# Kernel tuning notes

Measured on AMD Instinct MI355X. Metric: run time of the kernel, lower is better.

Reference implementation:

```python
import jax, jax.numpy as jnp
import numpy as np

N_EMBD = 1024
COND = 1024
N_HEAD = 16
B, N, NTOK = 4, 2048, 2048


def setup_inputs() -> dict:
    key = jax.random.key(0)
    ks = jax.random.split(key, 10)
    s = 0.02
    return {
        "x": jax.random.normal(ks[0], (B, N, N_EMBD), jnp.float32),
        "encoder_output": jax.random.normal(ks[1], (B, NTOK, COND), jnp.float32),
        "Wq": jax.random.normal(ks[2], (N_EMBD, N_EMBD), jnp.float32) * s,
        "bq": jnp.zeros((N_EMBD,), jnp.float32),
        "Wk": jax.random.normal(ks[3], (N_EMBD, COND), jnp.float32) * s,
        "bk": jnp.zeros((N_EMBD,), jnp.float32),
        "Wv": jax.random.normal(ks[4], (N_EMBD, COND), jnp.float32) * s,
        "bv": jnp.zeros((N_EMBD,), jnp.float32),
        "Wp": jax.random.normal(ks[5], (N_EMBD, N_EMBD), jnp.float32) * s,
        "bp": jnp.zeros((N_EMBD,), jnp.float32),
    }


def reference(x, encoder_output, Wq, bq, Wk, bk, Wv, bv, Wp, bp):
    Bx, Nx, C = x.shape
    H = N_HEAD
    D = C // H
    # projections (torch Linear: y = x @ W^T + b)
    q = (x @ Wq.T + bq).reshape(Bx, Nx, H, D)               # b n h d
    k = (encoder_output @ Wk.T + bk).reshape(Bx, -1, H, D)  # b t h d
    v = (encoder_output @ Wv.T + bv).reshape(Bx, -1, H, D)
    scale = 1.0 / jnp.sqrt(jnp.asarray(D, x.dtype))
    att = jnp.einsum("bnhd,bthd->bhnt", q, k) * scale
    att = jax.nn.softmax(att, axis=-1)
    y = jnp.einsum("bhnt,bthd->bnhd", att, v).reshape(Bx, Nx, C)
    y = y @ Wp.T + bp  # dropout is identity at inference (p effectively 0)
    return y
```

## Files before the change

kernel.cpp:

```cpp
#include <hip/hip_runtime.h>

typedef short bf16x8 __attribute__((ext_vector_type(8)));
typedef float f32x4 __attribute__((ext_vector_type(4)));
typedef unsigned int u32x2 __attribute__((ext_vector_type(2)));

#define AS1 __attribute__((address_space(1)))
#define AS3 __attribute__((address_space(3)))

__device__ __forceinline__ void gld16(void* lds, const void* g) {
  __builtin_amdgcn_global_load_lds((const AS1 unsigned int*)g,
                                   (AS3 unsigned int*)lds, 16, 0, 0);
}

__device__ __forceinline__ unsigned short f2bf(float f) {
  union { float f; unsigned int u; } c; c.f = f;
  return (unsigned short)((c.u + 0x7FFFu + ((c.u >> 16) & 1u)) >> 16);
}

__device__ __forceinline__ unsigned int cvtpk(float lo, float hi) {
  unsigned int r;
  asm("v_cvt_pk_bf16_f32 %0, %1, %2" : "=v"(r) : "v"(lo), "v"(hi));
  return r;
}

__global__ void cvt_kernel(const float4* __restrict__ in0,
                           const float4* __restrict__ in1,
                           ushort4* __restrict__ out0,
                           ushort4* __restrict__ out1, int n4) {
  const float4* in = blockIdx.y ? in1 : in0;
  ushort4* out = blockIdx.y ? out1 : out0;
  int i = blockIdx.x * blockDim.x + threadIdx.x;
  int stride = gridDim.x * blockDim.x;
  for (; i < n4; i += stride) {
    float4 v = in[i];
    ushort4 o;
    o.x = f2bf(v.x); o.y = f2bf(v.y); o.z = f2bf(v.z); o.w = f2bf(v.w);
    out[i] = o;
  }
}

__global__ void cvtw_kernel(const float4* w0, const float4* w1,
                            const float4* w2, const float4* w3,
                            ushort4* o0, ushort4* o1, ushort4* o2, ushort4* o3,
                            int n4) {
  const float4* in; ushort4* out;
  switch (blockIdx.y) {
    case 0: in = w0; out = o0; break;
    case 1: in = w1; out = o1; break;
    case 2: in = w2; out = o2; break;
    default: in = w3; out = o3; break;
  }
  int i = blockIdx.x * blockDim.x + threadIdx.x;
  int stride = gridDim.x * blockDim.x;
  for (; i < n4; i += stride) {
    float4 v = in[i];
    ushort4 o;
    o.x = f2bf(v.x); o.y = f2bf(v.y); o.z = f2bf(v.z); o.w = f2bf(v.w);
    out[i] = o;
  }
}

__global__ __launch_bounds__(256) void gemm_qkv_kernel(
    const unsigned short* __restrict__ Xb,
    const unsigned short* __restrict__ Eb,
    const unsigned short* __restrict__ Wqb,
    const unsigned short* __restrict__ Wkb,
    const unsigned short* __restrict__ Wvb,
    const float* __restrict__ bq,
    const float* __restrict__ bk,
    const float* __restrict__ bv,
    unsigned short* __restrict__ Qw,
    unsigned short* __restrict__ Kw,
    unsigned short* __restrict__ VTw,
    float qscale)
{
  __shared__ alignas(16) unsigned short As[2][4 * 128 * 8];
  __shared__ alignas(16) unsigned short Bs[2][4 * 128 * 8];

  const int sec = blockIdx.x >> 3;
  const int bx = blockIdx.x & 7;
  const unsigned short* A = (sec == 0) ? Xb : Eb;
  const unsigned short* W = (sec == 0) ? Wqb : (sec == 1) ? Wkb : Wvb;
  const float* bias = (sec == 0) ? bq : (sec == 1) ? bk : bv;

  const int K = 1024, N = 1024;
  const int tid = threadIdx.x;
  const int lane = tid & 63;
  const int w = tid >> 6;
  const int wr = (w >> 1) * 64;
  const int wc = (w & 1) * 64;
  const int lrow = lane & 15;
  const int lk = lane >> 4;
  const long m0 = (long)blockIdx.y * 128;
  const long n0 = (long)bx * 128;

  f32x4 acc[4][4] = {};

  const int c0 = tid, c1 = tid + 256;
  const unsigned short* Ag0 = A + (m0 + (c0 & 127)) * (long)K + (c0 >> 7) * 8;
  const unsigned short* Ag1 = A + (m0 + (c1 & 127)) * (long)K + (c1 >> 7) * 8;
  const unsigned short* Wg0 = W + (n0 + (c0 & 127)) * (long)K + (c0 >> 7) * 8;
  const unsigned short* Wg1 = W + (n0 + (c1 & 127)) * (long)K + (c1 >> 7) * 8;

  const int arow = wr + lrow;
  const int brow = wc + lrow;
  const int nt = K >> 5;

  gld16(As[0] + c0 * 8, Ag0);
  gld16(As[0] + c1 * 8, Ag1);
  gld16(Bs[0] + c0 * 8, Wg0);
  gld16(Bs[0] + c1 * 8, Wg1);

  int cur = 0;
  for (int t = 0; t < nt; ++t) {
    __syncthreads();
    if (t + 1 < nt) {
      const int kt = (t + 1) * 32;
      gld16(As[cur ^ 1] + c0 * 8, Ag0 + kt);
      gld16(As[cur ^ 1] + c1 * 8, Ag1 + kt);
      gld16(Bs[cur ^ 1] + c0 * 8, Wg0 + kt);
      gld16(Bs[cur ^ 1] + c1 * 8, Wg1 + kt);
    }
    const unsigned short* as = As[cur];
    const unsigned short* bs = Bs[cur];
    bf16x8 af[4], bfr[4];
#pragma unroll
    for (int i = 0; i < 4; ++i)
      af[i] = *(const bf16x8*)(as + (lk * 128 + arow + i * 16) * 8);
#pragma unroll
    for (int j = 0; j < 4; ++j)
      bfr[j] = *(const bf16x8*)(bs + (lk * 128 + brow + j * 16) * 8);
    if (sec != 2) {
#pragma unroll
      for (int i = 0; i < 4; ++i)
#pragma unroll
        for (int j = 0; j < 4; ++j)
          acc[i][j] = __builtin_amdgcn_mfma_f32_16x16x32_bf16(af[i], bfr[j], acc[i][j], 0, 0, 0);
    } else {
#pragma unroll
      for (int i = 0; i < 4; ++i)
#pragma unroll
        for (int j = 0; j < 4; ++j)
          acc[i][j] = __builtin_amdgcn_mfma_f32_16x16x32_bf16(bfr[i], af[j], acc[i][j], 0, 0, 0);
    }
    cur ^= 1;
  }

  if (sec != 2) {
    unsigned short* out = (sec == 0) ? Qw : Kw;
    const float scale = (sec == 0) ? qscale : 1.0f;
#pragma unroll
    for (int j = 0; j < 4; ++j) {
      const long col = n0 + wc + j * 16 + lrow;
      const float bv_ = bias[col];
#pragma unroll
      for (int i = 0; i < 4; ++i)
#pragma unroll
        for (int r = 0; r < 4; ++r) {
          const long row = m0 + wr + i * 16 + lk * 4 + r;
          out[row * (long)N + col] = f2bf((acc[i][j][r] + bv_) * scale);
        }
    }
  } else {
#pragma unroll
    for (int i = 0; i < 4; ++i)
#pragma unroll
      for (int r = 0; r < 4; ++r) {
        const long feat = n0 + wc + i * 16 + lk * 4 + r;
        const float bv_ = bias[feat];
#pragma unroll
        for (int j = 0; j < 4; ++j) {
          const long col = m0 + wr + j * 16 + lrow;
          VTw[feat * 8192 + col] = f2bf(acc[i][j][r] + bv_);
        }
      }
  }
}

__global__ __launch_bounds__(256) void gemm_bt_kernel(
    const unsigned short* __restrict__ A,
    const unsigned short* __restrict__ W,
    const float* __restrict__ bias,
    float* __restrict__ outF,
    int M, int N, int K)
{
  __shared__ alignas(16) unsigned short As[2][4 * 128 * 8];
  __shared__ alignas(16) unsigned short Bs[2][4 * 128 * 8];

  const int tid = threadIdx.x;
  const int lane = tid & 63;
  const int w = tid >> 6;
  const int wr = (w >> 1) * 64;
  const int wc = (w & 1) * 64;
  const int lrow = lane & 15;
  const int lk = lane >> 4;
  const long m0 = (long)blockIdx.y * 128;
  const long n0 = (long)blockIdx.x * 128;

  f32x4 acc[4][4] = {};

  const int c0 = tid, c1 = tid + 256;
  const unsigned short* Ag0 = A + (m0 + (c0 & 127)) * (long)K + (c0 >> 7) * 8;
  const unsigned short* Ag1 = A + (m0 + (c1 & 127)) * (long)K + (c1 >> 7) * 8;
  const unsigned short* Wg0 = W + (n0 + (c0 & 127)) * (long)K + (c0 >> 7) * 8;
  const unsigned short* Wg1 = W + (n0 + (c1 & 127)) * (long)K + (c1 >> 7) * 8;

  const int arow = wr + lrow;
  const int brow = wc + lrow;
  const int nt = K >> 5;

  gld16(As[0] + c0 * 8, Ag0);
  gld16(As[0] + c1 * 8, Ag1);
  gld16(Bs[0] + c0 * 8, Wg0);
  gld16(Bs[0] + c1 * 8, Wg1);

  int cur = 0;
  for (int t = 0; t < nt; ++t) {
    __syncthreads();
    if (t + 1 < nt) {
      const int kt = (t + 1) * 32;
      gld16(As[cur ^ 1] + c0 * 8, Ag0 + kt);
      gld16(As[cur ^ 1] + c1 * 8, Ag1 + kt);
      gld16(Bs[cur ^ 1] + c0 * 8, Wg0 + kt);
      gld16(Bs[cur ^ 1] + c1 * 8, Wg1 + kt);
    }
    const unsigned short* as = As[cur];
    const unsigned short* bs = Bs[cur];
    bf16x8 af[4], bfr[4];
#pragma unroll
    for (int i = 0; i < 4; ++i)
      af[i] = *(const bf16x8*)(as + (lk * 128 + arow + i * 16) * 8);
#pragma unroll
    for (int j = 0; j < 4; ++j)
      bfr[j] = *(const bf16x8*)(bs + (lk * 128 + brow + j * 16) * 8);
#pragma unroll
    for (int i = 0; i < 4; ++i)
#pragma unroll
      for (int j = 0; j < 4; ++j)
        acc[i][j] = __builtin_amdgcn_mfma_f32_16x16x32_bf16(af[i], bfr[j], acc[i][j], 0, 0, 0);
    cur ^= 1;
  }

#pragma unroll
  for (int j = 0; j < 4; ++j) {
    const long col = n0 + wc + j * 16 + lrow;
    const float bv_ = bias[col];
#pragma unroll
    for (int i = 0; i < 4; ++i)
#pragma unroll
      for (int r = 0; r < 4; ++r) {
        const long row = m0 + wr + i * 16 + lk * 4 + r;
        outF[row * (long)N + col] = acc[i][j][r] + bv_;
      }
  }
}

__global__ __launch_bounds__(256) void attn_kernel(
    const unsigned short* __restrict__ Q,
    const unsigned short* __restrict__ K,
    const unsigned short* __restrict__ VT,
    unsigned short* __restrict__ Y)
{
  __shared__ alignas(16) unsigned short Ks[2][8 * 64 * 8];
  __shared__ alignas(16) unsigned short Vt[2][64 * 64];
  __shared__ alignas(16) unsigned short Ps[128 * 72];

  const int tid = threadIdx.x;
  const int lane = tid & 63;
  const int w = tid >> 6;
  const int lrow = lane & 15;
  const int lk = lane >> 4;

  const int id = blockIdx.x;
  const int r8 = id & 7;
  const int s5 = id >> 3;
  const int qt = s5 & 15;
  const int bh = r8 + 8 * (s5 >> 4);
  const int h = bh & 15, b = bh >> 4;
  const long C = 1024, T = 2048, NQ = 2048;

  const unsigned short* Qg = Q + ((long)b * NQ + qt * 128) * C + h * 64;
  const unsigned short* Kg0 = K + (long)b * T * C + h * 64;
  const unsigned short* Vg0 = VT + (long)(h * 64) * 8192 + b * 2048;

  {
    int c = tid;
    gld16(Ks[0] + c * 8, Kg0 + (long)(c & 63) * C + (c >> 6) * 8);
    c = tid + 256;
    gld16(Ks[0] + c * 8, Kg0 + (long)(c & 63) * C + (c >> 6) * 8);
    c = tid;
    gld16(Vt[0] + c * 8, Vg0 + (long)(c >> 3) * 8192 + (((c & 7) ^ ((c >> 3) & 7)) * 8));
    c = tid + 256;
    gld16(Vt[0] + c * 8, Vg0 + (long)(c >> 3) * 8192 + (((c & 7) ^ ((c >> 3) & 7)) * 8));
  }
  bf16x8 qf[2][2];
#pragma unroll
  for (int f = 0; f < 2; ++f)
#pragma unroll
    for (int kk = 0; kk < 2; ++kk)
      qf[f][kk] = *(const bf16x8*)(Qg + (long)(f * 64 + w * 16 + lrow) * C + (kk * 4 + lk) * 8);

  bf16x8 ones;
#pragma unroll
  for (int e = 0; e < 8; ++e) ones[e] = (short)0x3F80;

  __syncthreads();

  f32x4 oA[4] = {}, oB[4] = {};
  f32x4 olA = {}, olB = {};
  float mrA = -1e30f, mrB = -1e30f;
  int cur = 0;

  const int qrow0 = w * 16 + lrow;

  for (int kt = 0; kt < (int)T; kt += 64) {
    const bool more = (kt + 64 < (int)T);
    if (more) {
      int c = tid;
      gld16(Ks[cur ^ 1] + c * 8, Kg0 + (long)(kt + 64 + (c & 63)) * C + (c >> 6) * 8);
      gld16(Vt[cur ^ 1] + c * 8,
            Vg0 + (long)(c >> 3) * 8192 + kt + 64 + (((c & 7) ^ ((c >> 3) & 7)) * 8));
      c = tid + 256;
      gld16(Ks[cur ^ 1] + c * 8, Kg0 + (long)(kt + 64 + (c & 63)) * C + (c >> 6) * 8);
      gld16(Vt[cur ^ 1] + c * 8,
            Vg0 + (long)(c >> 3) * 8192 + kt + 64 + (((c & 7) ^ ((c >> 3) & 7)) * 8));
    }

    f32x4 sA[4] = {}, sB[4] = {};
    __builtin_amdgcn_s_setprio(1);
#pragma unroll
    for (int kk = 0; kk < 2; ++kk) {
#pragma unroll
      for (int j = 0; j < 4; ++j) {
        bf16x8 kf = *(const bf16x8*)(Ks[cur] + ((kk * 4 + lk) * 64 + j * 16 + lrow) * 8);
        sA[j] = __builtin_amdgcn_mfma_f32_16x16x32_bf16(kf, qf[0][kk], sA[j], 0, 0, 0);
        sB[j] = __builtin_amdgcn_mfma_f32_16x16x32_bf16(kf, qf[1][kk], sB[j], 0, 0, 0);
      }
    }
    __builtin_amdgcn_s_setprio(0);

    float pmA, pmB;
    {
      float a = fmaxf(fmaxf(fmaxf(sA[0][0], sA[0][1]), fmaxf(sA[0][2], sA[0][3])),
                      fmaxf(fmaxf(sA[1][0], sA[1][1]), fmaxf(sA[1][2], sA[1][3])));
      float b2 = fmaxf(fmaxf(fmaxf(sA[2][0], sA[2][1]), fmaxf(sA[2][2], sA[2][3])),
                       fmaxf(fmaxf(sA[3][0], sA[3][1]), fmaxf(sA[3][2], sA[3][3])));
      pmA = fmaxf(a, b2);
      pmA = fmaxf(pmA, __shfl_xor(pmA, 16));
      pmA = fmaxf(pmA, __shfl_xor(pmA, 32));
      float c2 = fmaxf(fmaxf(fmaxf(sB[0][0], sB[0][1]), fmaxf(sB[0][2], sB[0][3])),
                       fmaxf(fmaxf(sB[1][0], sB[1][1]), fmaxf(sB[1][2], sB[1][3])));
      float d2 = fmaxf(fmaxf(fmaxf(sB[2][0], sB[2][1]), fmaxf(sB[2][2], sB[2][3])),
                       fmaxf(fmaxf(sB[3][0], sB[3][1]), fmaxf(sB[3][2], sB[3][3])));
      pmB = fmaxf(c2, d2);
      pmB = fmaxf(pmB, __shfl_xor(pmB, 16));
      pmB = fmaxf(pmB, __shfl_xor(pmB, 32));
    }
    if (__any(fmaxf(pmA - mrA, pmB - mrB) > 8.0f)) {
      {
        const float mn = fmaxf(mrA, pmA);
        const float al = __builtin_amdgcn_exp2f(mrA - mn);
        mrA = mn; olA *= al;
#pragma unroll
        for (int j = 0; j < 4; ++j) oA[j] *= al;
      }
      {
        const float mn = fmaxf(mrB, pmB);
        const float al = __builtin_amdgcn_exp2f(mrB - mn);
        mrB = mn; olB *= al;
#pragma unroll
        for (int j = 0; j < 4; ++j) oB[j] *= al;
      }
    }
#pragma unroll
    for (int j = 0; j < 4; ++j) {
      float p0 = __builtin_amdgcn_exp2f(sA[j][0] - mrA);
      float p1 = __builtin_amdgcn_exp2f(sA[j][1] - mrA);
      float p2 = __builtin_amdgcn_exp2f(sA[j][2] - mrA);
      float p3 = __builtin_amdgcn_exp2f(sA[j][3] - mrA);
      u32x2 pk;
      pk.x = cvtpk(p0, p1);
      pk.y = cvtpk(p2, p3);
      *(u32x2*)(Ps + qrow0 * 72 + j * 16 + lk * 4) = pk;
    }
#pragma unroll
    for (int j = 0; j < 4; ++j) {
      float p0 = __builtin_amdgcn_exp2f(sB[j][0] - mrB);
      float p1 = __builtin_amdgcn_exp2f(sB[j][1] - mrB);
      float p2 = __builtin_amdgcn_exp2f(sB[j][2] - mrB);
      float p3 = __builtin_amdgcn_exp2f(sB[j][3] - mrB);
      u32x2 pk;
      pk.x = cvtpk(p0, p1);
      pk.y = cvtpk(p2, p3);
      *(u32x2*)(Ps + (64 + qrow0) * 72 + j * 16 + lk * 4) = pk;
    }

    const unsigned short* vt = Vt[cur];
    __builtin_amdgcn_s_setprio(1);
#pragma unroll
    for (int kk = 0; kk < 2; ++kk) {
      bf16x8 pa0 = *(const bf16x8*)(Ps + qrow0 * 72 + kk * 32 + lk * 8);
      bf16x8 pa1 = *(const bf16x8*)(Ps + (64 + qrow0) * 72 + kk * 32 + lk * 8);
      olA = __builtin_amdgcn_mfma_f32_16x16x32_bf16(ones, pa0, olA, 0, 0, 0);
      olB = __builtin_amdgcn_mfma_f32_16x16x32_bf16(ones, pa1, olB, 0, 0, 0);
#pragma unroll
      for (int j = 0; j < 4; ++j) {
        const int d = j * 16 + lrow;
        bf16x8 vb = *(const bf16x8*)(vt + d * 64 + ((((kk * 4 + lk) ^ (d & 7)) & 7) << 3));
        oA[j] = __builtin_amdgcn_mfma_f32_16x16x32_bf16(vb, pa0, oA[j], 0, 0, 0);
        oB[j] = __builtin_amdgcn_mfma_f32_16x16x32_bf16(vb, pa1, oB[j], 0, 0, 0);
      }
    }
    __builtin_amdgcn_s_setprio(0);

    cur ^= 1;
    __syncthreads();
  }

  unsigned short* Yg = Y + ((long)b * NQ + qt * 128) * C + h * 64;
  const float linvA = 1.f / olA[0];
  const float linvB = 1.f / olB[0];
#pragma unroll
  for (int j = 0; j < 4; ++j) {
    u32x2 pk;
    pk.x = cvtpk(oA[j][0] * linvA, oA[j][1] * linvA);
    pk.y = cvtpk(oA[j][2] * linvA, oA[j][3] * linvA);
    *(u32x2*)(Yg + (long)qrow0 * C + j * 16 + lk * 4) = pk;
    pk.x = cvtpk(oB[j][0] * linvB, oB[j][1] * linvB);
    pk.y = cvtpk(oB[j][2] * linvB, oB[j][3] * linvB);
    *(u32x2*)(Yg + (long)(64 + qrow0) * C + j * 16 + lk * 4) = pk;
  }
}

extern "C" void kernel_launch(void* const* d_in, const int* in_sizes, int n_in,
                              void* d_out, int out_size, void* d_ws, size_t ws_size,
                              hipStream_t stream) {
  (void)in_sizes; (void)n_in; (void)out_size; (void)ws_size;
  const float* x   = (const float*)d_in[0];
  const float* enc = (const float*)d_in[1];
  const float* Wq  = (const float*)d_in[2];
  const float* bq  = (const float*)d_in[3];
  const float* Wk  = (const float*)d_in[4];
  const float* bk  = (const float*)d_in[5];
  const float* Wv  = (const float*)d_in[6];
  const float* bv  = (const float*)d_in[7];
  const float* Wp  = (const float*)d_in[8];
  const float* bp  = (const float*)d_in[9];

  const long M = 4L * 2048;
  const long C = 1024;

  char* ws = (char*)d_ws;
  size_t off = 0;
  auto alloc = [&](size_t bytes) {
    char* p = ws + off;
    off += (bytes + 255) & ~(size_t)255;
    return p;
  };
  unsigned short* Xb  = (unsigned short*)alloc(M * C * 2);
  unsigned short* Eb  = (unsigned short*)alloc(M * C * 2);
  unsigned short* Wqb = (unsigned short*)alloc(C * C * 2);
  unsigned short* Wkb = (unsigned short*)alloc(C * C * 2);
  unsigned short* Wvb = (unsigned short*)alloc(C * C * 2);
  unsigned short* Wpb = (unsigned short*)alloc(C * C * 2);
  unsigned short* Qw  = (unsigned short*)alloc(M * C * 2);
  unsigned short* Kw  = (unsigned short*)alloc(M * C * 2);
  unsigned short* VTw = (unsigned short*)alloc(M * C * 2);
  unsigned short* Yb  = (unsigned short*)alloc(M * C * 2);

  {
    int n4 = (int)(M * C / 4);
    int blocks = (n4 + 255) / 256; if (blocks > 2048) blocks = 2048;
    cvt_kernel<<<dim3(blocks, 2), 256, 0, stream>>>(
        (const float4*)x, (const float4*)enc, (ushort4*)Xb, (ushort4*)Eb, n4);
    int w4 = (int)(C * C / 4);
    cvtw_kernel<<<dim3(1024, 4), 256, 0, stream>>>(
        (const float4*)Wq, (const float4*)Wk, (const float4*)Wv, (const float4*)Wp,
        (ushort4*)Wqb, (ushort4*)Wkb, (ushort4*)Wvb, (ushort4*)Wpb, w4);
  }

  const float qscale = 0.125f * 1.44269504088896f;
  gemm_qkv_kernel<<<dim3(24, 64), 256, 0, stream>>>(
      Xb, Eb, Wqb, Wkb, Wvb, bq, bk, bv, Qw, Kw, VTw, qscale);

  attn_kernel<<<1024, 256, 0, stream>>>(Qw, Kw, VTw, Yb);

  gemm_bt_kernel<<<dim3(8, 64), 256, 0, stream>>>(
      Yb, Wpb, bp, (float*)d_out, (int)M, (int)C, (int)C);
}
```

Measured before the change: 298.6 us.

## Enlarge GEMM tiles to 256x128 with 512 threads, fold max offset into scores

Both projection GEMMs now use 512-thread blocks computing 256x128 output tiles, so each weight tile is reused across twice as many rows and fewer blocks are launched. The attention kernel initialises score accumulators with the negated running max, which removes the per-element subtraction before exp2, and tracks max increments as deltas. The bf16 epilogue conversion uses the hardware pack instruction instead of integer rounding. Larger tiles raise shared-memory use and halve the block count, which may hurt occupancy or load balance.

```diff
diff --git a/kernel.cpp b/kernel.cpp
--- a/kernel.cpp
+++ b/kernel.cpp
@@ -15,6 +15,12 @@
 __device__ __forceinline__ unsigned short f2bf(float f) {
   union { float f; unsigned int u; } c; c.f = f;
   return (unsigned short)((c.u + 0x7FFFu + ((c.u >> 16) & 1u)) >> 16);
+}
+
+__device__ __forceinline__ unsigned short cvt1(float x) {
+  unsigned int r;
+  asm("v_cvt_pk_bf16_f32 %0, %1, %1" : "=v"(r) : "v"(x));
+  return (unsigned short)r;
 }
 
 __device__ __forceinline__ unsigned int cvtpk(float lo, float hi) {
@@ -60,7 +66,7 @@
   }
 }
 
-__global__ __launch_bounds__(256) void gemm_qkv_kernel(
+__global__ __launch_bounds__(512) void gemm_qkv_kernel(
     const unsigned short* __restrict__ Xb,
     const unsigned short* __restrict__ Eb,
     const unsigned short* __restrict__ Wqb,
@@ -74,11 +80,11 @@
     unsigned short* __restrict__ VTw,
     float qscale)
 {
-  __shared__ alignas(16) unsigned short As[2][4 * 128 * 8];
+  __shared__ alignas(16) unsigned short As[2][4 * 256 * 8];
   __shared__ alignas(16) unsigned short Bs[2][4 * 128 * 8];
 
   const int sec = blockIdx.x >> 3;
-  const int bx = blockIdx.x & 7;
+  const int nx = blockIdx.x & 7;
   const unsigned short* A = (sec == 0) ? Xb : Eb;
   const unsigned short* W = (sec == 0) ? Wqb : (sec == 1) ? Wkb : Wvb;
   const float* bias = (sec == 0) ? bq : (sec == 1) ? bk : bv;
@@ -91,45 +97,40 @@
   const int wc = (w & 1) * 64;
   const int lrow = lane & 15;
   const int lk = lane >> 4;
-  const long m0 = (long)blockIdx.y * 128;
-  const long n0 = (long)bx * 128;
+  const long m0 = (long)blockIdx.y * 256;
+  const long n0 = (long)nx * 128;
 
   f32x4 acc[4][4] = {};
 
-  const int c0 = tid, c1 = tid + 256;
-  const unsigned short* Ag0 = A + (m0 + (c0 & 127)) * (long)K + (c0 >> 7) * 8;
-  const unsigned short* Ag1 = A + (m0 + (c1 & 127)) * (long)K + (c1 >> 7) * 8;
-  const unsigned short* Wg0 = W + (n0 + (c0 & 127)) * (long)K + (c0 >> 7) * 8;
-  const unsigned short* Wg1 = W + (n0 + (c1 & 127)) * (long)K + (c1 >> 7) * 8;
-
-  const int arow = wr + lrow;
-  const int brow = wc + lrow;
+  const int ca0 = tid, ca1 = tid + 512, cb = tid;
+  const unsigned short* Ag0 = A + (m0 + (ca0 & 255)) * (long)K + (ca0 >> 8) * 8;
+  const unsigned short* Ag1 = A + (m0 + (ca1 & 255)) * (long)K + (ca1 >> 8) * 8;
+  const unsigned short* Wg0 = W + (n0 + (cb & 127)) * (long)K + (cb >> 7) * 8;
+
   const int nt = K >> 5;
 
-  gld16(As[0] + c0 * 8, Ag0);
-  gld16(As[0] + c1 * 8, Ag1);
-  gld16(Bs[0] + c0 * 8, Wg0);
-  gld16(Bs[0] + c1 * 8, Wg1);
+  gld16(As[0] + ca0 * 8, Ag0);
+  gld16(As[0] + ca1 * 8, Ag1);
+  gld16(Bs[0] + cb * 8, Wg0);
 
   int cur = 0;
   for (int t = 0; t < nt; ++t) {
     __syncthreads();
     if (t + 1 < nt) {
       const int kt = (t + 1) * 32;
-      gld16(As[cur ^ 1] + c0 * 8, Ag0 + kt);
-      gld16(As[cur ^ 1] + c1 * 8, Ag1 + kt);
-      gld16(Bs[cur ^ 1] + c0 * 8, Wg0 + kt);
-      gld16(Bs[cur ^ 1] + c1 * 8, Wg1 + kt);
+      gld16(As[cur ^ 1] + ca0 * 8, Ag0 + kt);
+      gld16(As[cur ^ 1] + ca1 * 8, Ag1 + kt);
+      gld16(Bs[cur ^ 1] + cb * 8, Wg0 + kt);
     }
     const unsigned short* as = As[cur];
     const unsigned short* bs = Bs[cur];
     bf16x8 af[4], bfr[4];
 #pragma unroll
     for (int i = 0; i < 4; ++i)
-      af[i] = *(const bf16x8*)(as + (lk * 128 + arow + i * 16) * 8);
+      af[i] = *(const bf16x8*)(as + (lk * 256 + wr + lrow + i * 16) * 8);
 #pragma unroll
     for (int j = 0; j < 4; ++j)
-      bfr[j] = *(const bf16x8*)(bs + (lk * 128 + brow + j * 16) * 8);
+      bfr[j] = *(const bf16x8*)(bs + (lk * 128 + wc + lrow + j * 16) * 8);
     if (sec != 2) {
 #pragma unroll
       for (int i = 0; i < 4; ++i)
@@ -158,7 +159,7 @@
 #pragma unroll
         for (int r = 0; r < 4; ++r) {
           const long row = m0 + wr + i * 16 + lk * 4 + r;
-          out[row * (long)N + col] = f2bf((acc[i][j][r] + bv_) * scale);
+          out[row * (long)N + col] = cvt1((acc[i][j][r] + bv_) * scale);
         }
     }
   } else {
@@ -171,22 +172,22 @@
 #pragma unroll
         for (int j = 0; j < 4; ++j) {
           const long col = m0 + wr + j * 16 + lrow;
-          VTw[feat * 8192 + col] = f2bf(acc[i][j][r] + bv_);
+          VTw[feat * 8192 + col] = cvt1(acc[i][j][r] + bv_);
         }
       }
   }
 }
 
-__global__ __launch_bounds__(256) void gemm_bt_kernel(
+__global__ __launch_bounds__(512) void gemm_p_kernel(
     const unsigned short* __restrict__ A,
     const unsigned short* __restrict__ W,
     const float* __restrict__ bias,
-    float* __restrict__ outF,
-    int M, int N, int K)
+    float* __restrict__ outF)
 {
-  __shared__ alignas(16) unsigned short As[2][4 * 128 * 8];
+  __shared__ alignas(16) unsigned short As[2][4 * 256 * 8];
   __shared__ alignas(16) unsigned short Bs[2][4 * 128 * 8];
 
+  const int K = 1024, N = 1024;
   const int tid = threadIdx.x;
   const int lane = tid & 63;
   const int w = tid >> 6;
@@ -194,45 +195,40 @@
   const int wc = (w & 1) * 64;
   const int lrow = lane & 15;
   const int lk = lane >> 4;
-  const long m0 = (long)blockIdx.y * 128;
+  const long m0 = (long)blockIdx.y * 256;
   const long n0 = (long)blockIdx.x * 128;
 
   f32x4 acc[4][4] = {};
 
-  const int c0 = tid, c1 = tid + 256;
-  const unsigned short* Ag0 = A + (m0 + (c0 & 127)) * (long)K + (c0 >> 7) * 8;
-  const unsigned short* Ag1 = A + (m0 + (c1 & 127)) * (long)K + (c1 >> 7) * 8;
-  const unsigned short* Wg0 = W + (n0 + (c0 & 127)) * (long)K + (c0 >> 7) * 8;
-  const unsigned short* Wg1 = W + (n0 + (c1 & 127)) * (long)K + (c1 >> 7) * 8;
-
-  const int arow = wr + lrow;
-  const int brow = wc + lrow;
+  const int ca0 = tid, ca1 = tid + 512, cb = tid;
+  const unsigned short* Ag0 = A + (m0 + (ca0 & 255)) * (long)K + (ca0 >> 8) * 8;
+  const unsigned short* Ag1 = A + (m0 + (ca1 & 255)) * (long)K + (ca1 >> 8) * 8;
+  const unsigned short* Wg0 = W + (n0 + (cb & 127)) * (long)K + (cb >> 7) * 8;
+
   const int nt = K >> 5;
 
-  gld16(As[0] + c0 * 8, Ag0);
-  gld16(As[0] + c1 * 8, Ag1);
-  gld16(Bs[0] + c0 * 8, Wg0);
-  gld16(Bs[0] + c1 * 8, Wg1);
+  gld16(As[0] + ca0 * 8, Ag0);
+  gld16(As[0] + ca1 * 8, Ag1);
+  gld16(Bs[0] + cb * 8, Wg0);
 
   int cur = 0;
   for (int t = 0; t < nt; ++t) {
     __syncthreads();
     if (t + 1 < nt) {
       const int kt = (t + 1) * 32;
-      gld16(As[cur ^ 1] + c0 * 8, Ag0 + kt);
-      gld16(As[cur ^ 1] + c1 * 8, Ag1 + kt);
-      gld16(Bs[cur ^ 1] + c0 * 8, Wg0 + kt);
-      gld16(Bs[cur ^ 1] + c1 * 8, Wg1 + kt);
+      gld16(As[cur ^ 1] + ca0 * 8, Ag0 + kt);
+      gld16(As[cur ^ 1] + ca1 * 8, Ag1 + kt);
+      gld16(Bs[cur ^ 1] + cb * 8, Wg0 + kt);
     }
     const unsigned short* as = As[cur];
     const unsigned short* bs = Bs[cur];
     bf16x8 af[4], bfr[4];
 #pragma unroll
     for (int i = 0; i < 4; ++i)
-      af[i] = *(const bf16x8*)(as + (lk * 128 + arow + i * 16) * 8);
+      af[i] = *(const bf16x8*)(as + (lk * 256 + wr + lrow + i * 16) * 8);
 #pragma unroll
     for (int j = 0; j < 4; ++j)
-      bfr[j] = *(const bf16x8*)(bs + (lk * 128 + brow + j * 16) * 8);
+      bfr[j] = *(const bf16x8*)(bs + (lk * 128 + wc + lrow + j * 16) * 8);
 #pragma unroll
     for (int i = 0; i < 4; ++i)
 #pragma unroll
@@ -308,7 +304,7 @@
 
   f32x4 oA[4] = {}, oB[4] = {};
   f32x4 olA = {}, olB = {};
-  float mrA = -1e30f, mrB = -1e30f;
+  float mrA = 0.f, mrB = 0.f;
   int cur = 0;
 
   const int qrow0 = w * 16 + lrow;
@@ -326,7 +322,12 @@
             Vg0 + (long)(c >> 3) * 8192 + kt + 64 + (((c & 7) ^ ((c >> 3) & 7)) * 8));
     }
 
-    f32x4 sA[4] = {}, sB[4] = {};
+    f32x4 sA[4], sB[4];
+#pragma unroll
+    for (int j = 0; j < 4; ++j)
+#pragma unroll
+      for (int r = 0; r < 4; ++r) { sA[j][r] = -mrA; sB[j][r] = -mrB; }
+
     __builtin_amdgcn_s_setprio(1);
 #pragma unroll
     for (int kk = 0; kk < 2; ++kk) {
@@ -356,28 +357,27 @@
       pmB = fmaxf(pmB, __shfl_xor(pmB, 16));
       pmB = fmaxf(pmB, __shfl_xor(pmB, 32));
     }
-    if (__any(fmaxf(pmA - mrA, pmB - mrB) > 8.0f)) {
-      {
-        const float mn = fmaxf(mrA, pmA);
-        const float al = __builtin_amdgcn_exp2f(mrA - mn);
-        mrA = mn; olA *= al;
-#pragma unroll
-        for (int j = 0; j < 4; ++j) oA[j] *= al;
+    if (__any(fmaxf(pmA, pmB) > 8.0f)) {
+      const float dmA = fmaxf(pmA, 0.f);
+      const float alA = __builtin_amdgcn_exp2f(-dmA);
+      mrA += dmA; olA *= alA;
+      const float dmB = fmaxf(pmB, 0.f);
+      const float alB = __builtin_amdgcn_exp2f(-dmB);
+      mrB += dmB; olB *= alB;
+#pragma unroll
+      for (int j = 0; j < 4; ++j) {
+        oA[j] *= alA;
+        oB[j] *= alB;
+#pragma unroll
+        for (int r = 0; r < 4; ++r) { sA[j][r] -= dmA; sB[j][r] -= dmB; }
       }
-      {
-        const float mn = fmaxf(mrB, pmB);
-        const float al = __builtin_amdgcn_exp2f(mrB - mn);
-        mrB = mn; olB *= al;
-#pragma unroll
-        for (int j = 0; j < 4; ++j) oB[j] *= al;
-      }
     }
 #pragma unroll
     for (int j = 0; j < 4; ++j) {
-      float p0 = __builtin_amdgcn_exp2f(sA[j][0] - mrA);
-      float p1 = __builtin_amdgcn_exp2f(sA[j][1] - mrA);
-      float p2 = __builtin_amdgcn_exp2f(sA[j][2] - mrA);
-      float p3 = __builtin_amdgcn_exp2f(sA[j][3] - mrA);
+      float p0 = __builtin_amdgcn_exp2f(sA[j][0]);
+      float p1 = __builtin_amdgcn_exp2f(sA[j][1]);
+      float p2 = __builtin_amdgcn_exp2f(sA[j][2]);
+      float p3 = __builtin_amdgcn_exp2f(sA[j][3]);
       u32x2 pk;
       pk.x = cvtpk(p0, p1);
       pk.y = cvtpk(p2, p3);
@@ -385,10 +385,10 @@
     }
 #pragma unroll
     for (int j = 0; j < 4; ++j) {
-      float p0 = __builtin_amdgcn_exp2f(sB[j][0] - mrB);
-      float p1 = __builtin_amdgcn_exp2f(sB[j][1] - mrB);
-      float p2 = __builtin_amdgcn_exp2f(sB[j][2] - mrB);
-      float p3 = __builtin_amdgcn_exp2f(sB[j][3] - mrB);
+      float p0 = __builtin_amdgcn_exp2f(sB[j][0]);
+      float p1 = __builtin_amdgcn_exp2f(sB[j][1]);
+      float p2 = __builtin_amdgcn_exp2f(sB[j][2]);
+      float p3 = __builtin_amdgcn_exp2f(sB[j][3]);
       u32x2 pk;
       pk.x = cvtpk(p0, p1);
       pk.y = cvtpk(p2, p3);
@@ -480,11 +480,10 @@
   }
 
   const float qscale = 0.125f * 1.44269504088896f;
-  gemm_qkv_kernel<<<dim3(24, 64), 256, 0, stream>>>(
+  gemm_qkv_kernel<<<dim3(24, 32), 512, 0, stream>>>(
       Xb, Eb, Wqb, Wkb, Wvb, bq, bk, bv, Qw, Kw, VTw, qscale);
 
   attn_kernel<<<1024, 256, 0, stream>>>(Qw, Kw, VTw, Yb);
 
-  gemm_bt_kernel<<<dim3(8, 64), 256, 0, stream>>>(
-      Yb, Wpb, bp, (float*)d_out, (int)M, (int)C, (int)C);
-}
+  gemm_p_kernel<<<dim3(8, 32), 512, 0, stream>>>(Yb, Wpb, bp, (float*)d_out);
+}
```

After: 329.6 us. +10.4%, slower.

## Remap GEMM blocks per XCD, fold running max into MFMA init, use hardware bf16 convert

Applied to the files above, without the earlier changes.

Both GEMMs now launch a 1D grid and remap the block id so that consecutive ids dealt to the same XCD cover neighbouring tiles, aiming for better L2 reuse. The output projection is specialised with compile-time K and N. In attention, the S accumulators start at -max so the MFMA applies the subtraction, and the rescale becomes a delta update, removing per-element subtracts from the exp path. Epilogue bf16 rounding switches from the integer f2bf routine to the v_cvt_pk_bf16_f32 instruction. Together these touch several unrelated parts, and the changed max bookkeeping could affect numerics if it is wrong.

```diff
diff --git a/kernel.cpp b/kernel.cpp
--- a/kernel.cpp
+++ b/kernel.cpp
@@ -15,6 +15,12 @@
 __device__ __forceinline__ unsigned short f2bf(float f) {
   union { float f; unsigned int u; } c; c.f = f;
   return (unsigned short)((c.u + 0x7FFFu + ((c.u >> 16) & 1u)) >> 16);
+}
+
+__device__ __forceinline__ unsigned short cvt1(float x) {
+  unsigned int r;
+  asm("v_cvt_pk_bf16_f32 %0, %1, %1" : "=v"(r) : "v"(x));
+  return (unsigned short)r;
 }
 
 __device__ __forceinline__ unsigned int cvtpk(float lo, float hi) {
@@ -77,8 +83,13 @@
   __shared__ alignas(16) unsigned short As[2][4 * 128 * 8];
   __shared__ alignas(16) unsigned short Bs[2][4 * 128 * 8];
 
-  const int sec = blockIdx.x >> 3;
-  const int bx = blockIdx.x & 7;
+  const int bid = blockIdx.x;
+  const int o = (bid & 7) * 192 + (bid >> 3);
+  const int xx = o % 24;
+  const int yy = o / 24;
+  const int sec = xx >> 3;
+  const int nx = xx & 7;
+
   const unsigned short* A = (sec == 0) ? Xb : Eb;
   const unsigned short* W = (sec == 0) ? Wqb : (sec == 1) ? Wkb : Wvb;
   const float* bias = (sec == 0) ? bq : (sec == 1) ? bk : bv;
@@ -91,8 +102,8 @@
   const int wc = (w & 1) * 64;
   const int lrow = lane & 15;
   const int lk = lane >> 4;
-  const long m0 = (long)blockIdx.y * 128;
-  const long n0 = (long)bx * 128;
+  const long m0 = (long)yy * 128;
+  const long n0 = (long)nx * 128;
 
   f32x4 acc[4][4] = {};
 
@@ -158,7 +169,7 @@
 #pragma unroll
         for (int r = 0; r < 4; ++r) {
           const long row = m0 + wr + i * 16 + lk * 4 + r;
-          out[row * (long)N + col] = f2bf((acc[i][j][r] + bv_) * scale);
+          out[row * (long)N + col] = cvt1((acc[i][j][r] + bv_) * scale);
         }
     }
   } else {
@@ -171,22 +182,27 @@
 #pragma unroll
         for (int j = 0; j < 4; ++j) {
           const long col = m0 + wr + j * 16 + lrow;
-          VTw[feat * 8192 + col] = f2bf(acc[i][j][r] + bv_);
+          VTw[feat * 8192 + col] = cvt1(acc[i][j][r] + bv_);
         }
       }
   }
 }
 
-__global__ __launch_bounds__(256) void gemm_bt_kernel(
+__global__ __launch_bounds__(256) void gemm_p_kernel(
     const unsigned short* __restrict__ A,
     const unsigned short* __restrict__ W,
     const float* __restrict__ bias,
-    float* __restrict__ outF,
-    int M, int N, int K)
+    float* __restrict__ outF)
 {
   __shared__ alignas(16) unsigned short As[2][4 * 128 * 8];
   __shared__ alignas(16) unsigned short Bs[2][4 * 128 * 8];
 
+  const int bid = blockIdx.x;
+  const int o = (bid & 7) * 64 + (bid >> 3);
+  const int nx = o & 7;
+  const int yy = o >> 3;
+
+  const int K = 1024, N = 1024;
   const int tid = threadIdx.x;
   const int lane = tid & 63;
   const int w = tid >> 6;
@@ -194,8 +210,8 @@
   const int wc = (w & 1) * 64;
   const int lrow = lane & 15;
   const int lk = lane >> 4;
-  const long m0 = (long)blockIdx.y * 128;
-  const long n0 = (long)blockIdx.x * 128;
+  const long m0 = (long)yy * 128;
+  const long n0 = (long)nx * 128;
 
   f32x4 acc[4][4] = {};
 
@@ -308,7 +324,7 @@
 
   f32x4 oA[4] = {}, oB[4] = {};
   f32x4 olA = {}, olB = {};
-  float mrA = -1e30f, mrB = -1e30f;
+  float mrA = 0.f, mrB = 0.f;
   int cur = 0;
 
   const int qrow0 = w * 16 + lrow;
@@ -326,7 +342,12 @@
             Vg0 + (long)(c >> 3) * 8192 + kt + 64 + (((c & 7) ^ ((c >> 3) & 7)) * 8));
     }
 
-    f32x4 sA[4] = {}, sB[4] = {};
+    f32x4 sA[4], sB[4];
+#pragma unroll
+    for (int j = 0; j < 4; ++j)
+#pragma unroll
+      for (int r = 0; r < 4; ++r) { sA[j][r] = -mrA; sB[j][r] = -mrB; }
+
     __builtin_amdgcn_s_setprio(1);
 #pragma unroll
     for (int kk = 0; kk < 2; ++kk) {
@@ -356,28 +377,27 @@
       pmB = fmaxf(pmB, __shfl_xor(pmB, 16));
       pmB = fmaxf(pmB, __shfl_xor(pmB, 32));
     }
-    if (__any(fmaxf(pmA - mrA, pmB - mrB) > 8.0f)) {
-      {
-        const float mn = fmaxf(mrA, pmA);
-        const float al = __builtin_amdgcn_exp2f(mrA - mn);
-        mrA = mn; olA *= al;
-#pragma unroll
-        for (int j = 0; j < 4; ++j) oA[j] *= al;
+    if (__any(fmaxf(pmA, pmB) > 8.0f)) {
+      const float dmA = fmaxf(pmA, 0.f);
+      const float alA = __builtin_amdgcn_exp2f(-dmA);
+      mrA += dmA; olA *= alA;
+      const float dmB = fmaxf(pmB, 0.f);
+      const float alB = __builtin_amdgcn_exp2f(-dmB);
+      mrB += dmB; olB *= alB;
+#pragma unroll
+      for (int j = 0; j < 4; ++j) {
+        oA[j] *= alA;
+        oB[j] *= alB;
+#pragma unroll
+        for (int r = 0; r < 4; ++r) { sA[j][r] -= dmA; sB[j][r] -= dmB; }
       }
-      {
-        const float mn = fmaxf(mrB, pmB);
-        const float al = __builtin_amdgcn_exp2f(mrB - mn);
-        mrB = mn; olB *= al;
-#pragma unroll
-        for (int j = 0; j < 4; ++j) oB[j] *= al;
-      }
     }
 #pragma unroll
     for (int j = 0; j < 4; ++j) {
-      float p0 = __builtin_amdgcn_exp2f(sA[j][0] - mrA);
-      float p1 = __builtin_amdgcn_exp2f(sA[j][1] - mrA);
-      float p2 = __builtin_amdgcn_exp2f(sA[j][2] - mrA);
-      float p3 = __builtin_amdgcn_exp2f(sA[j][3] - mrA);
+      float p0 = __builtin_amdgcn_exp2f(sA[j][0]);
+      float p1 = __builtin_amdgcn_exp2f(sA[j][1]);
+      float p2 = __builtin_amdgcn_exp2f(sA[j][2]);
+      float p3 = __builtin_amdgcn_exp2f(sA[j][3]);
       u32x2 pk;
       pk.x = cvtpk(p0, p1);
       pk.y = cvtpk(p2, p3);
@@ -385,10 +405,10 @@
     }
 #pragma unroll
     for (int j = 0; j < 4; ++j) {
-      float p0 = __builtin_amdgcn_exp2f(sB[j][0] - mrB);
-      float p1 = __builtin_amdgcn_exp2f(sB[j][1] - mrB);
-      float p2 = __builtin_amdgcn_exp2f(sB[j][2] - mrB);
-      float p3 = __builtin_amdgcn_exp2f(sB[j][3] - mrB);
+      float p0 = __builtin_amdgcn_exp2f(sB[j][0]);
+      float p1 = __builtin_amdgcn_exp2f(sB[j][1]);
+      float p2 = __builtin_amdgcn_exp2f(sB[j][2]);
+      float p3 = __builtin_amdgcn_exp2f(sB[j][3]);
       u32x2 pk;
       pk.x = cvtpk(p0, p1);
       pk.y = cvtpk(p2, p3);
@@ -480,11 +500,10 @@
   }
 
   const float qscale = 0.125f * 1.44269504088896f;
-  gemm_qkv_kernel<<<dim3(24, 64), 256, 0, stream>>>(
+  gemm_qkv_kernel<<<1536, 256, 0, stream>>>(
       Xb, Eb, Wqb, Wkb, Wvb, bq, bk, bv, Qw, Kw, VTw, qscale);
 
   attn_kernel<<<1024, 256, 0, stream>>>(Qw, Kw, VTw, Yb);
 
-  gemm_bt_kernel<<<dim3(8, 64), 256, 0, stream>>>(
-      Yb, Wpb, bp, (float*)d_out, (int)M, (int)C, (int)C);
-}
+  gemm_p_kernel<<<512, 256, 0, stream>>>(Yb, Wpb, bp, (float*)d_out);
+}
```

Measured after the change: 292.2 us. 1.02x faster.
